# Performance work log

Measured on AMD Instinct MI355X. Metric: run time of the kernel, lower is better.

The kernel has to match this reference:

```python
import jax, jax.numpy as jnp
import numpy as np

N, E, D_IN, H, D_OUT = 50000, 1600000, 256, 128, 64


def setup_inputs() -> dict:
    key = jax.random.key(0)
    ks = jax.random.split(key, 8)
    x = jax.random.normal(ks[0], (N, D_IN), dtype=jnp.float32)
    edge_index = jax.random.randint(ks[1], (2, E), 0, N, dtype=jnp.int64)
    W1 = jax.random.normal(ks[2], (D_IN, H), dtype=jnp.float32) / np.float32(np.sqrt(D_IN))
    b1 = jnp.zeros((H,), jnp.float32)
    W2 = jax.random.normal(ks[3], (H, H), dtype=jnp.float32) / np.float32(np.sqrt(H))
    b2 = jnp.zeros((H,), jnp.float32)
    W3 = jax.random.normal(ks[4], (H, D_OUT), dtype=jnp.float32) / np.float32(np.sqrt(H))
    b3 = jnp.zeros((D_OUT,), jnp.float32)
    return {"x": x, "W1": W1, "b1": b1, "W2": W2, "b2": b2, "W3": W3, "b3": b3,
            "edge_index": edge_index}


def reference(x, W1, b1, W2, b2, W3, b3, edge_index):
    n = x.shape[0]
    # GCN: add self-loops, symmetric normalization D^{-1/2}(A+I)D^{-1/2}
    loop = jnp.arange(n, dtype=edge_index.dtype)
    src = jnp.concatenate([edge_index[0], loop])
    dst = jnp.concatenate([edge_index[1], loop])
    deg = jax.ops.segment_sum(jnp.ones_like(dst, x.dtype), dst, num_segments=n)
    dinv = jnp.where(deg > 0, jax.lax.rsqrt(deg), 0.0).astype(x.dtype)
    norm = dinv[src] * dinv[dst]  # [E+N]

    def gcn_layer(h, W, b):
        h = h @ W                                   # [N, F_out]
        msg = norm[:, None] * h[src]                # gather + scale, [E+N, F_out]
        return jax.ops.segment_sum(msg, dst, num_segments=n) + b

    h = jax.nn.relu(gcn_layer(x, W1, b1))
    h = jax.nn.relu(gcn_layer(h, W2, b2))
    return gcn_layer(h, W3, b3)
```

## Files before the change

### kernel.cpp

```cpp
#include <hip/hip_runtime.h>


constexpr int DIN = 256;
constexpr int HID = 128;
constexpr int DOUT = 64;
constexpr int MAXB = 1024;
constexpr int BSH = 6;
constexpr int EPB = 8192;

typedef unsigned short ushort_t;
typedef unsigned int uint_t;
typedef __attribute__((ext_vector_type(8))) short bf16x8;
typedef __attribute__((ext_vector_type(4))) float f32x4;

__device__ inline ushort_t f2bf(float f) {
  uint_t u = __float_as_uint(f);
  u += 0x7FFF + ((u >> 16) & 1);
  return (ushort_t)(u >> 16);
}
__device__ inline float bf2f(ushort_t b) {
  return __uint_as_float(((uint_t)b) << 16);
}

template <int SH>
__device__ inline uint_t ldrow32(const ushort_t* __restrict__ t, int c, uint_t lb) {
  return *(const uint_t*)((const char*)t + ((((uint_t)c) << SH) | lb));
}
__device__ inline float ldf32(const float* __restrict__ p, int c) {
  return *(const float*)((const char*)p + (((uint_t)c) << 2));
}


__device__ inline void wprep_one(const float* __restrict__ W, ushort_t* __restrict__ Bhi,
                                 ushort_t* __restrict__ Blo, int K, int F, int i) {
  int k = i / F, nn = i % F;
  int t = nn >> 4, s = k >> 5, q = (k >> 3) & 3, j = k & 7;
  int lane = q * 16 + (nn & 15);
  int KS = K >> 5;
  size_t idx = (((size_t)t * KS + s) * 64 + (size_t)lane) * 8 + j;
  float w = W[i];
  ushort_t h = f2bf(w);
  float r = w - bf2f(h);
  Bhi[idx] = h;
  Blo[idx] = f2bf(r);
}


__global__ __launch_bounds__(256) void initprep_kernel(
    int* __restrict__ bucket_total, int iblocks,
    const float* __restrict__ W1, ushort_t* __restrict__ W1hi, ushort_t* __restrict__ W1lo,
    const float* __restrict__ W2, ushort_t* __restrict__ W2hi, ushort_t* __restrict__ W2lo,
    const float* __restrict__ W3, ushort_t* __restrict__ W3hi, ushort_t* __restrict__ W3lo) {
  if ((int)blockIdx.x < iblocks) {
    int i = blockIdx.x * 256 + threadIdx.x;
    if (i < MAXB) bucket_total[i] = 0;
  } else {
    int idx = ((int)blockIdx.x - iblocks) * 256 + threadIdx.x;
    constexpr int S1 = DIN * HID;
    constexpr int S2 = S1 + HID * HID;
    constexpr int S3 = S2 + HID * DOUT;
    if (idx < S1) wprep_one(W1, W1hi, W1lo, DIN, HID, idx);
    else if (idx < S2) wprep_one(W2, W2hi, W2lo, HID, HID, idx - S1);
    else if (idx < S3) wprep_one(W3, W3hi, W3lo, HID, DOUT, idx - S2);
  }
}


__global__ __launch_bounds__(256) void bin_kernel(const int* __restrict__ dst, int e,
    int nbuckets, int* __restrict__ bucket_total, int* __restrict__ block_base) {
  __shared__ int h[MAXB];
  int tid = threadIdx.x;
  for (int i = tid; i < nbuckets; i += 256) h[i] = 0;
  __syncthreads();
  int base = blockIdx.x * EPB;
  int end = min(base + EPB, e);
  for (int i = base + tid; i < end; i += 256) atomicAdd(&h[dst[i] >> BSH], 1);
  __syncthreads();
  for (int i = tid; i < nbuckets; i += 256) {
    int v = h[i];
    if (v) block_base[(size_t)blockIdx.x * nbuckets + i] = atomicAdd(&bucket_total[i], v);
  }
}


__global__ __launch_bounds__(256) void scan_buckets_kernel(const int* __restrict__ total,
    int* __restrict__ base, int nb) {
  __shared__ int sums[256];
  int t = threadIdx.x;
  int a[4];
  int ls = 0;
#pragma unroll
  for (int k = 0; k < 4; ++k) {
    int idx = t * 4 + k;
    a[k] = (idx < nb) ? total[idx] : 0;
    ls += a[k];
  }
  sums[t] = ls;
  __syncthreads();
  for (int off = 1; off < 256; off <<= 1) {
    int u = (t >= off) ? sums[t - off] : 0;
    __syncthreads();
    sums[t] += u;
    __syncthreads();
  }
  int run = sums[t] - ls;
#pragma unroll
  for (int k = 0; k < 4; ++k) {
    int idx = t * 4 + k;
    if (idx < nb) base[idx] = run;
    run += a[k];
  }
  if (t == 255) base[nb] = sums[255];
}


template <int K, int F, bool SCALE>
__device__ inline void gemm_mfma_dev(const float* __restrict__ X,
    const ushort_t* __restrict__ Bhi, const ushort_t* __restrict__ Blo,
    const float* __restrict__ dinv, ushort_t* __restrict__ T, int n, int bid) {
  constexpr int NT = F / 16;
  constexpr int KS = K / 32;
  int wave = threadIdx.x >> 6;
  int lane = threadIdx.x & 63;
  int q = lane >> 4;
  int m = lane & 15;
  int arow = bid * 64 + wave * 16 + m;
  bool valid = arow < n;
  const float* xrow = X + (size_t)arow * K;

  f32x4 acc[NT];
#pragma unroll
  for (int t = 0; t < NT; ++t) acc[t] = (f32x4){0.f, 0.f, 0.f, 0.f};

  for (int s = 0; s < KS; ++s) {
    float av[8];
    if (valid) {
      float4 u0 = *(const float4*)(xrow + s * 32 + q * 8);
      float4 u1 = *(const float4*)(xrow + s * 32 + q * 8 + 4);
      av[0] = u0.x; av[1] = u0.y; av[2] = u0.z; av[3] = u0.w;
      av[4] = u1.x; av[5] = u1.y; av[6] = u1.z; av[7] = u1.w;
    } else {
#pragma unroll
      for (int j = 0; j < 8; ++j) av[j] = 0.f;
    }
    bf16x8 ahi, alo;
#pragma unroll
    for (int j = 0; j < 8; ++j) {
      ushort_t h = f2bf(av[j]);
      ahi[j] = (short)h;
      alo[j] = (short)f2bf(av[j] - bf2f(h));
    }
#pragma unroll
    for (int t = 0; t < NT; ++t) {
      size_t boff = (((size_t)t * KS + s) * 64 + (size_t)lane) * 8;
      bf16x8 bh = *(const bf16x8*)(Bhi + boff);
      bf16x8 bl = *(const bf16x8*)(Blo + boff);
      acc[t] = __builtin_amdgcn_mfma_f32_16x16x32_bf16(ahi, bh, acc[t], 0, 0, 0);
      acc[t] = __builtin_amdgcn_mfma_f32_16x16x32_bf16(alo, bh, acc[t], 0, 0, 0);
      acc[t] = __builtin_amdgcn_mfma_f32_16x16x32_bf16(ahi, bl, acc[t], 0, 0, 0);
    }
  }

  int orow_base = bid * 64 + wave * 16 + q * 4;
#pragma unroll
  for (int r = 0; r < 4; ++r) {
    int orow = orow_base + r;
    if (orow >= n) continue;
    float sc = SCALE ? dinv[orow] : 1.0f;
    ushort_t* trow = T + (size_t)orow * F + m;
#pragma unroll
    for (int t = 0; t < NT; ++t) trow[t * 16] = f2bf(sc * acc[t][r]);
  }
}


__global__ __launch_bounds__(256) void fusedA2_kernel(
    const float* __restrict__ X, const ushort_t* __restrict__ Bhi,
    const ushort_t* __restrict__ Blo, ushort_t* __restrict__ T, int n, int gblocks,
    const int* __restrict__ src, const int* __restrict__ dst,
    const int* __restrict__ bucket_base, const int* __restrict__ block_base,
    uint_t* __restrict__ binned, int e, int nbuckets) {
  if ((int)blockIdx.x < gblocks) {
    gemm_mfma_dev<DIN, HID, false>(X, Bhi, Blo, nullptr, T, n, blockIdx.x);
  } else {
    __shared__ int rkh[MAXB];
    __shared__ int cbase[MAXB];
    int tid = threadIdx.x;
    int blk = (int)blockIdx.x - gblocks;
    for (int i = tid; i < nbuckets; i += 256) {
      rkh[i] = 0;
      cbase[i] = bucket_base[i] + block_base[(size_t)blk * nbuckets + i];
    }
    __syncthreads();
    int base = blk * EPB;
    int end = min(base + EPB, e);
    for (int i = base + tid; i < end; i += 256) {
      int d = dst[i];
      int s = src[i];
      int b = d >> BSH;
      int r = atomicAdd(&rkh[b], 1);
      binned[cbase[b] + r] = ((uint_t)d << 16) | (uint_t)s;
    }
  }
}


__global__ __launch_bounds__(256) void csr_kernel(const uint_t* __restrict__ binned,
    const int* __restrict__ bucket_base, int n, int* __restrict__ row_start,
    int* __restrict__ deg, float* __restrict__ dinv, int* __restrict__ col) {
  __shared__ int cnt[64];
  __shared__ int rk[64];
  __shared__ int rs[64];
  __shared__ int ebs[2];
  int tid = threadIdx.x;
  int b = blockIdx.x;
  int node0 = b << BSH;
  if (tid < 64) { cnt[tid] = 0; rk[tid] = 0; }
  if (tid == 0) { ebs[0] = bucket_base[b]; ebs[1] = bucket_base[b + 1]; }
  __syncthreads();
  int ebase = ebs[0];
  int esz = ebs[1] - ebase;
  for (int i = tid; i < esz; i += 256)
    atomicAdd(&cnt[(int)(binned[ebase + i] >> 16) - node0], 1);
  __syncthreads();
  if (tid < 64) {
    int v = cnt[tid];
    int inc = v;
#pragma unroll
    for (int off = 1; off < 64; off <<= 1) {
      int u = __shfl_up(inc, off, 64);
      if (tid >= off) inc += u;
    }
    rs[tid] = inc - v;
    int node = node0 + tid;
    if (node < n) {
      deg[node] = v + 1;
      dinv[node] = rsqrtf((float)(v + 1));
      row_start[node] = ebase + (inc - v);
    }
  }
  __syncthreads();
  for (int i = tid; i < esz; i += 256) {
    uint_t p = binned[ebase + i];
    int l = (int)(p >> 16) - node0;
    int r = atomicAdd(&rk[l], 1);
    col[ebase + rs[l] + r] = (int)(p & 0xFFFFu);
  }
}


template <int FOUT, bool GD>
__global__ __launch_bounds__(256) void spmm_gemm_kernel(
    const ushort_t* __restrict__ t, const int* __restrict__ row_start,
    const int* __restrict__ deg, const int* __restrict__ col,
    const float* __restrict__ dinv, const float* __restrict__ bias,
    const ushort_t* __restrict__ Bhi, const ushort_t* __restrict__ Blo,
    ushort_t* __restrict__ Tout, int n) {
  constexpr int FIN = 128;
  constexpr int NPB = 8;
  constexpr int LDW = FIN + 4;
  __shared__ float agg[16][LDW];
  int wave = threadIdx.x >> 6;
  int lane = threadIdx.x & 63;
  int tid = threadIdx.x;
  int nb0 = (int)blockIdx.x * NPB;
  uint_t lb = (uint_t)lane << 2;

  {
    float* z = &agg[8][0];
    for (int i = tid; i < 8 * LDW; i += 256) z[i] = 0.f;
  }

  {
    int ln0 = wave * 2;
    int n0 = nb0 + ln0;
    int n1 = n0 + 1;
    bool h0 = n0 < n, h1 = n1 < n;
    int rs0 = h0 ? row_start[n0] : 0, e0 = h0 ? deg[n0] - 1 : 0;
    int rs1 = h1 ? row_start[n1] : 0, e1 = h1 ? deg[n1] - 1 : 0;
    float di0 = h0 ? dinv[n0] : 0.f;
    float di1 = h1 ? dinv[n1] : 0.f;
    float bx = bias[2 * lane], by = bias[2 * lane + 1];
    float ax0 = 0.f, ay0 = 0.f, ax1 = 0.f, ay1 = 0.f;
    if (h0) {
      uint_t s0 = ldrow32<8>(t, n0, lb);
      ax0 = bf2f((ushort_t)(s0 & 0xFFFF)); ay0 = bf2f((ushort_t)(s0 >> 16));
      if constexpr (GD) { ax0 *= di0; ay0 *= di0; }
    }
    if (h1) {
      uint_t s1 = ldrow32<8>(t, n1, lb);
      ax1 = bf2f((ushort_t)(s1 & 0xFFFF)); ay1 = bf2f((ushort_t)(s1 >> 16));
      if constexpr (GD) { ax1 *= di1; ay1 *= di1; }
    }
    int p0 = rs0, q0 = rs0 + e0;
    int p1 = rs1, q1 = rs1 + e1;
    while (p0 + 4 <= q0 && p1 + 4 <= q1) {
      int c[8];
      uint_t v[8];
      float dc[8];
#pragma unroll
      for (int j = 0; j < 4; ++j) { c[j] = col[p0 + j]; c[4 + j] = col[p1 + j]; }
#pragma unroll
      for (int j = 0; j < 8; ++j) {
        v[j] = ldrow32<8>(t, c[j], lb);
        if constexpr (GD) dc[j] = ldf32(dinv, c[j]);
      }
#pragma unroll
      for (int j = 0; j < 4; ++j) {
        if constexpr (GD) {
          ax0 = fmaf(dc[j], bf2f((ushort_t)(v[j] & 0xFFFF)), ax0);
          ay0 = fmaf(dc[j], bf2f((ushort_t)(v[j] >> 16)), ay0);
          ax1 = fmaf(dc[4 + j], bf2f((ushort_t)(v[4 + j] & 0xFFFF)), ax1);
          ay1 = fmaf(dc[4 + j], bf2f((ushort_t)(v[4 + j] >> 16)), ay1);
        } else {
          ax0 += bf2f((ushort_t)(v[j] & 0xFFFF));
          ay0 += bf2f((ushort_t)(v[j] >> 16));
          ax1 += bf2f((ushort_t)(v[4 + j] & 0xFFFF));
          ay1 += bf2f((ushort_t)(v[4 + j] >> 16));
        }
      }
      p0 += 4; p1 += 4;
    }
    for (; p0 + 4 <= q0; p0 += 4) {
      int c[4]; uint_t v[4]; float dc[4];
#pragma unroll
      for (int j = 0; j < 4; ++j) c[j] = col[p0 + j];
#pragma unroll
      for (int j = 0; j < 4; ++j) {
        v[j] = ldrow32<8>(t, c[j], lb);
        if constexpr (GD) dc[j] = ldf32(dinv, c[j]);
      }
#pragma unroll
      for (int j = 0; j < 4; ++j) {
        if constexpr (GD) {
          ax0 = fmaf(dc[j], bf2f((ushort_t)(v[j] & 0xFFFF)), ax0);
          ay0 = fmaf(dc[j], bf2f((ushort_t)(v[j] >> 16)), ay0);
        } else {
          ax0 += bf2f((ushort_t)(v[j] & 0xFFFF)); ay0 += bf2f((ushort_t)(v[j] >> 16));
        }
      }
    }
    for (; p0 < q0; ++p0) {
      int c = col[p0];
      uint_t v = ldrow32<8>(t, c, lb);
      if constexpr (GD) {
        float d = ldf32(dinv, c);
        ax0 = fmaf(d, bf2f((ushort_t)(v & 0xFFFF)), ax0);
        ay0 = fmaf(d, bf2f((ushort_t)(v >> 16)), ay0);
      } else {
        ax0 += bf2f((ushort_t)(v & 0xFFFF)); ay0 += bf2f((ushort_t)(v >> 16));
      }
    }
    for (; p1 + 4 <= q1; p1 += 4) {
      int c[4]; uint_t v[4]; float dc[4];
#pragma unroll
      for (int j = 0; j < 4; ++j) c[j] = col[p1 + j];
#pragma unroll
      for (int j = 0; j < 4; ++j) {
        v[j] = ldrow32<8>(t, c[j], lb);
        if constexpr (GD) dc[j] = ldf32(dinv, c[j]);
      }
#pragma unroll
      for (int j = 0; j < 4; ++j) {
        if constexpr (GD) {
          ax1 = fmaf(dc[j], bf2f((ushort_t)(v[j] & 0xFFFF)), ax1);
          ay1 = fmaf(dc[j], bf2f((ushort_t)(v[j] >> 16)), ay1);
        } else {
          ax1 += bf2f((ushort_t)(v[j] & 0xFFFF)); ay1 += bf2f((ushort_t)(v[j] >> 16));
        }
      }
    }
    for (; p1 < q1; ++p1) {
      int c = col[p1];
      uint_t v = ldrow32<8>(t, c, lb);
      if constexpr (GD) {
        float d = ldf32(dinv, c);
        ax1 = fmaf(d, bf2f((ushort_t)(v & 0xFFFF)), ax1);
        ay1 = fmaf(d, bf2f((ushort_t)(v >> 16)), ay1);
      } else {
        ax1 += bf2f((ushort_t)(v & 0xFFFF)); ay1 += bf2f((ushort_t)(v >> 16));
      }
    }
    float2 o0, o1;
    o0.x = h0 ? fmaxf(fmaf(di0, ax0, bx), 0.f) : 0.f;
    o0.y = h0 ? fmaxf(fmaf(di0, ay0, by), 0.f) : 0.f;
    o1.x = h1 ? fmaxf(fmaf(di1, ax1, bx), 0.f) : 0.f;
    o1.y = h1 ? fmaxf(fmaf(di1, ay1, by), 0.f) : 0.f;
    *(float2*)&agg[ln0][2 * lane] = o0;
    *(float2*)&agg[ln0 + 1][2 * lane] = o1;
  }
  __syncthreads();

  constexpr int NT = FOUT / 16;
  constexpr int KS = FIN / 32;
  constexpr int NTW = NT / 4;
  int q = lane >> 4, m = lane & 15;
  f32x4 acc[NTW];
#pragma unroll
  for (int tt = 0; tt < NTW; ++tt) acc[tt] = (f32x4){0.f, 0.f, 0.f, 0.f};
  const float* arow = &agg[m][0];
#pragma unroll
  for (int s = 0; s < KS; ++s) {
    float4 u0 = *(const float4*)(arow + s * 32 + q * 8);
    float4 u1 = *(const float4*)(arow + s * 32 + q * 8 + 4);
    float av[8];
    av[0] = u0.x; av[1] = u0.y; av[2] = u0.z; av[3] = u0.w;
    av[4] = u1.x; av[5] = u1.y; av[6] = u1.z; av[7] = u1.w;
    bf16x8 ahi, alo;
#pragma unroll
    for (int j = 0; j < 8; ++j) {
      ushort_t h = f2bf(av[j]);
      ahi[j] = (short)h;
      alo[j] = (short)f2bf(av[j] - bf2f(h));
    }
#pragma unroll
    for (int tt = 0; tt < NTW; ++tt) {
      int tg = wave * NTW + tt;
      size_t boff = (((size_t)tg * KS + s) * 64 + (size_t)lane) * 8;
      bf16x8 bh = *(const bf16x8*)(Bhi + boff);
      bf16x8 bl = *(const bf16x8*)(Blo + boff);
      acc[tt] = __builtin_amdgcn_mfma_f32_16x16x32_bf16(ahi, bh, acc[tt], 0, 0, 0);
      acc[tt] = __builtin_amdgcn_mfma_f32_16x16x32_bf16(alo, bh, acc[tt], 0, 0, 0);
      acc[tt] = __builtin_amdgcn_mfma_f32_16x16x32_bf16(ahi, bl, acc[tt], 0, 0, 0);
    }
  }
#pragma unroll
  for (int r = 0; r < 4; ++r) {
    int row = q * 4 + r;
    if (row >= NPB) continue;
    int orow = nb0 + row;
    if (orow >= n) continue;
    float sc = dinv[orow];
    ushort_t* trow = Tout + (size_t)orow * FOUT + m;
#pragma unroll
    for (int tt = 0; tt < NTW; ++tt)
      trow[(wave * NTW + tt) * 16] = f2bf(sc * acc[tt][r]);
  }
}


__global__ __launch_bounds__(256) void spmm64_kernel(const ushort_t* __restrict__ t,
    const int* __restrict__ row_start, const int* __restrict__ deg,
    const int* __restrict__ col, const float* __restrict__ dinv,
    const float* __restrict__ bias, float* __restrict__ out, int n) {
  int gw = (int)((blockIdx.x * 256u + threadIdx.x) >> 6);
  int lane = threadIdx.x & 63;
  int half = lane >> 5;
  int hl = lane & 31;
  int n0 = gw * 2;
  if (n0 >= n) return;
  int node = n0 + half;
  bool valid = node < n;
  int vnode = valid ? node : n0;
  int rs = row_start[vnode];
  int e  = valid ? (deg[vnode] - 1) : 0;
  float di = dinv[vnode];
  uint_t lb = (uint_t)hl << 2;

  uint_t su = ldrow32<7>(t, vnode, lb);
  float ax = bf2f((ushort_t)(su & 0xFFFF));
  float ay = bf2f((ushort_t)(su >> 16));

  int emax = max(e, __shfl_xor(e, 32));
  for (int k = 0; k < emax; k += 4) {
    int c[4];
    uint_t v[4];
#pragma unroll
    for (int j = 0; j < 4; ++j) {
      int on = (k + j) < e;
      c[j] = col[on ? (rs + k + j) : 0];
    }
#pragma unroll
    for (int j = 0; j < 4; ++j) v[j] = ldrow32<7>(t, c[j], lb);
#pragma unroll
    for (int j = 0; j < 4; ++j) {
      if ((k + j) < e) {
        ax += bf2f((ushort_t)(v[j] & 0xFFFF));
        ay += bf2f((ushort_t)(v[j] >> 16));
      }
    }
  }
  if (valid) {
    float bx = bias[2 * hl], by = bias[2 * hl + 1];
    ax = fmaf(di, ax, bx);
    ay = fmaf(di, ay, by);
    float2 o;
    o.x = ax;
    o.y = ay;
    *(float2*)(out + (size_t)node * DOUT + 2 * hl) = o;
  }
}


extern "C" void kernel_launch(void* const* d_in, const int* in_sizes, int n_in,
                              void* d_out, int out_size, void* d_ws, size_t ws_size,
                              hipStream_t stream) {
  const float* x  = (const float*)d_in[0];
  const float* W1 = (const float*)d_in[1];
  const float* b1 = (const float*)d_in[2];
  const float* W2 = (const float*)d_in[3];
  const float* b2 = (const float*)d_in[4];
  const float* W3 = (const float*)d_in[5];
  const float* b3 = (const float*)d_in[6];
  const int* ei   = (const int*)d_in[7];

  int n = in_sizes[0] / DIN;
  int e = in_sizes[7] / 2;
  const int* src = ei;
  const int* dst = ei + e;

  char* ws = (char*)d_ws;
  size_t off = 0;
  auto alloc = [&](size_t bytes) -> void* {
    off = (off + 255) & ~(size_t)255;
    void* p = ws + off;
    off += bytes;
    return p;
  };
  int nbuckets = (n + 63) >> BSH;
  int nbin = (e + EPB - 1) / EPB;

  int*      bucket_total = (int*)alloc((size_t)MAXB * 4);
  int*      bucket_base  = (int*)alloc((size_t)(MAXB + 1) * 4);
  int*      block_base   = (int*)alloc((size_t)nbin * nbuckets * 4);
  uint_t*   binned       = (uint_t*)alloc((size_t)e * 4);
  int*      deg          = (int*)alloc((size_t)n * 4);
  float*    dinv         = (float*)alloc((size_t)n * 4);
  int*      row_start    = (int*)alloc((size_t)n * 4);
  int*      col          = (int*)alloc((size_t)e * 4);
  ushort_t* Ta           = (ushort_t*)alloc((size_t)n * HID * 2);
  ushort_t* Tb           = (ushort_t*)alloc((size_t)n * HID * 2);
  ushort_t* W1hi         = (ushort_t*)alloc((size_t)DIN * HID * 2);
  ushort_t* W1lo         = (ushort_t*)alloc((size_t)DIN * HID * 2);
  ushort_t* W2hi         = (ushort_t*)alloc((size_t)HID * HID * 2);
  ushort_t* W2lo         = (ushort_t*)alloc((size_t)HID * HID * 2);
  ushort_t* W3hi         = (ushort_t*)alloc((size_t)HID * DOUT * 2);
  ushort_t* W3lo         = (ushort_t*)alloc((size_t)HID * DOUT * 2);
  (void)ws_size;

  int gemm_blocks = (n + 63) / 64;
  int sg_blocks = (n + 7) / 8;
  int nwaves = (n + 1) / 2;
  int spmm_blocks = (nwaves + 3) / 4;
  constexpr int WPREP_TOTAL = DIN * HID + HID * HID + HID * DOUT;
  int wblocks = (WPREP_TOTAL + 255) / 256;
  int iblocks = MAXB / 256;

  initprep_kernel<<<iblocks + wblocks, 256, 0, stream>>>(
      bucket_total, iblocks,
      W1, W1hi, W1lo, W2, W2hi, W2lo, W3, W3hi, W3lo);
  bin_kernel<<<nbin, 256, 0, stream>>>(dst, e, nbuckets, bucket_total, block_base);
  scan_buckets_kernel<<<1, 256, 0, stream>>>(bucket_total, bucket_base, nbuckets);
  fusedA2_kernel<<<gemm_blocks + nbin, 256, 0, stream>>>(
      x, W1hi, W1lo, Ta, n, gemm_blocks,
      src, dst, bucket_base, block_base, binned, e, nbuckets);
  csr_kernel<<<nbuckets, 256, 0, stream>>>(binned, bucket_base, n, row_start, deg, dinv, col);

  spmm_gemm_kernel<HID, true><<<sg_blocks, 256, 0, stream>>>(
      Ta, row_start, deg, col, dinv, b1, W2hi, W2lo, Tb, n);
  spmm_gemm_kernel<DOUT, false><<<sg_blocks, 256, 0, stream>>>(
      Tb, row_start, deg, col, dinv, b2, W3hi, W3lo, Ta, n);
  spmm64_kernel<<<spmm_blocks, 256, 0, stream>>>(
      Ta, row_start, deg, col, dinv, b3, (float*)d_out, n);
}
```

Measured before the change: 356.8 us.

## Prescale layer-1 features by dinv in CSR kernel and deepen gather unrolling

The CSR build kernel now also multiplies each row of the first-layer transformed features (bf16) by its node's dinv, writing back in place. This removes the per-edge dinv gather from the first SpMM, so the GD template path goes away. The SpMM loops also gain an 8-wide paired unroll, and the final SpMM drops the lockstep half-wave loop in favour of per-node trip counts with 8 loads in flight. The tradeoff is an extra read/write pass over the layer-1 features and one additional bf16 rounding of the prescaled values.

```diff
diff --git a/kernel.cpp b/kernel.cpp
--- a/kernel.cpp
+++ b/kernel.cpp
@@ -25,9 +25,6 @@
 template <int SH>
 __device__ inline uint_t ldrow32(const ushort_t* __restrict__ t, int c, uint_t lb) {
   return *(const uint_t*)((const char*)t + ((((uint_t)c) << SH) | lb));
-}
-__device__ inline float ldf32(const float* __restrict__ p, int c) {
-  return *(const float*)((const char*)p + (((uint_t)c) << 2));
 }
 
 
@@ -207,10 +204,12 @@
 
 __global__ __launch_bounds__(256) void csr_kernel(const uint_t* __restrict__ binned,
     const int* __restrict__ bucket_base, int n, int* __restrict__ row_start,
-    int* __restrict__ deg, float* __restrict__ dinv, int* __restrict__ col) {
+    int* __restrict__ deg, float* __restrict__ dinv, int* __restrict__ col,
+    ushort_t* __restrict__ Ta) {
   __shared__ int cnt[64];
   __shared__ int rk[64];
   __shared__ int rs[64];
+  __shared__ float sdinv[64];
   __shared__ int ebs[2];
   int tid = threadIdx.x;
   int b = blockIdx.x;
@@ -232,10 +231,12 @@
       if (tid >= off) inc += u;
     }
     rs[tid] = inc - v;
+    float di = rsqrtf((float)(v + 1));
+    sdinv[tid] = di;
     int node = node0 + tid;
     if (node < n) {
       deg[node] = v + 1;
-      dinv[node] = rsqrtf((float)(v + 1));
+      dinv[node] = di;
       row_start[node] = ebase + (inc - v);
     }
   }
@@ -246,10 +247,28 @@
     int r = atomicAdd(&rk[l], 1);
     col[ebase + rs[l] + r] = (int)(p & 0xFFFFu);
   }
-}
-
-
-template <int FOUT, bool GD>
+  int nrows = min(64, n - node0);
+  if (nrows > 0) {
+    uint4* tw = (uint4*)Ta + ((size_t)node0 << 4);
+    int nv4 = nrows << 4;
+    for (int i = tid; i < nv4; i += 256) {
+      float sc = sdinv[i >> 4];
+      uint4 w = tw[i];
+      uint_t ww[4] = {w.x, w.y, w.z, w.w};
+#pragma unroll
+      for (int j = 0; j < 4; ++j) {
+        float lo = sc * bf2f((ushort_t)(ww[j] & 0xFFFF));
+        float hi = sc * bf2f((ushort_t)(ww[j] >> 16));
+        ww[j] = (uint_t)f2bf(lo) | ((uint_t)f2bf(hi) << 16);
+      }
+      w.x = ww[0]; w.y = ww[1]; w.z = ww[2]; w.w = ww[3];
+      tw[i] = w;
+    }
+  }
+}
+
+
+template <int FOUT>
 __global__ __launch_bounds__(256) void spmm_gemm_kernel(
     const ushort_t* __restrict__ t, const int* __restrict__ row_start,
     const int* __restrict__ deg, const int* __restrict__ col,
@@ -285,101 +304,74 @@
     if (h0) {
       uint_t s0 = ldrow32<8>(t, n0, lb);
       ax0 = bf2f((ushort_t)(s0 & 0xFFFF)); ay0 = bf2f((ushort_t)(s0 >> 16));
-      if constexpr (GD) { ax0 *= di0; ay0 *= di0; }
     }
     if (h1) {
       uint_t s1 = ldrow32<8>(t, n1, lb);
       ax1 = bf2f((ushort_t)(s1 & 0xFFFF)); ay1 = bf2f((ushort_t)(s1 >> 16));
-      if constexpr (GD) { ax1 *= di1; ay1 *= di1; }
     }
     int p0 = rs0, q0 = rs0 + e0;
     int p1 = rs1, q1 = rs1 + e1;
+    while (p0 + 8 <= q0 && p1 + 8 <= q1) {
+      int c[16];
+      uint_t v[16];
+#pragma unroll
+      for (int j = 0; j < 8; ++j) { c[j] = col[p0 + j]; c[8 + j] = col[p1 + j]; }
+#pragma unroll
+      for (int j = 0; j < 16; ++j) v[j] = ldrow32<8>(t, c[j], lb);
+#pragma unroll
+      for (int j = 0; j < 8; ++j) {
+        ax0 += bf2f((ushort_t)(v[j] & 0xFFFF));
+        ay0 += bf2f((ushort_t)(v[j] >> 16));
+        ax1 += bf2f((ushort_t)(v[8 + j] & 0xFFFF));
+        ay1 += bf2f((ushort_t)(v[8 + j] >> 16));
+      }
+      p0 += 8; p1 += 8;
+    }
     while (p0 + 4 <= q0 && p1 + 4 <= q1) {
       int c[8];
       uint_t v[8];
-      float dc[8];
 #pragma unroll
       for (int j = 0; j < 4; ++j) { c[j] = col[p0 + j]; c[4 + j] = col[p1 + j]; }
 #pragma unroll
-      for (int j = 0; j < 8; ++j) {
-        v[j] = ldrow32<8>(t, c[j], lb);
-        if constexpr (GD) dc[j] = ldf32(dinv, c[j]);
-      }
+      for (int j = 0; j < 8; ++j) v[j] = ldrow32<8>(t, c[j], lb);
 #pragma unroll
       for (int j = 0; j < 4; ++j) {
-        if constexpr (GD) {
-          ax0 = fmaf(dc[j], bf2f((ushort_t)(v[j] & 0xFFFF)), ax0);
-          ay0 = fmaf(dc[j], bf2f((ushort_t)(v[j] >> 16)), ay0);
-          ax1 = fmaf(dc[4 + j], bf2f((ushort_t)(v[4 + j] & 0xFFFF)), ax1);
-          ay1 = fmaf(dc[4 + j], bf2f((ushort_t)(v[4 + j] >> 16)), ay1);
-        } else {
-          ax0 += bf2f((ushort_t)(v[j] & 0xFFFF));
-          ay0 += bf2f((ushort_t)(v[j] >> 16));
-          ax1 += bf2f((ushort_t)(v[4 + j] & 0xFFFF));
-          ay1 += bf2f((ushort_t)(v[4 + j] >> 16));
-        }
+        ax0 += bf2f((ushort_t)(v[j] & 0xFFFF));
+        ay0 += bf2f((ushort_t)(v[j] >> 16));
+        ax1 += bf2f((ushort_t)(v[4 + j] & 0xFFFF));
+        ay1 += bf2f((ushort_t)(v[4 + j] >> 16));
       }
       p0 += 4; p1 += 4;
     }
     for (; p0 + 4 <= q0; p0 += 4) {
-      int c[4]; uint_t v[4]; float dc[4];
+      int c[4]; uint_t v[4];
 #pragma unroll
       for (int j = 0; j < 4; ++j) c[j] = col[p0 + j];
 #pragma unroll
+      for (int j = 0; j < 4; ++j) v[j] = ldrow32<8>(t, c[j], lb);
+#pragma unroll
       for (int j = 0; j < 4; ++j) {
-        v[j] = ldrow32<8>(t, c[j], lb);
-        if constexpr (GD) dc[j] = ldf32(dinv, c[j]);
+        ax0 += bf2f((ushort_t)(v[j] & 0xFFFF)); ay0 += bf2f((ushort_t)(v[j] >> 16));
       }
+    }
+    for (; p0 < q0; ++p0) {
+      uint_t v = ldrow32<8>(t, col[p0], lb);
+      ax0 += bf2f((ushort_t)(v & 0xFFFF)); ay0 += bf2f((ushort_t)(v >> 16));
+    }
+    for (; p1 + 4 <= q1; p1 += 4) {
+      int c[4]; uint_t v[4];
+#pragma unroll
+      for (int j = 0; j < 4; ++j) c[j] = col[p1 + j];
+#pragma unroll
+      for (int j = 0; j < 4; ++j) v[j] = ldrow32<8>(t, c[j], lb);
 #pragma unroll
       for (int j = 0; j < 4; ++j) {
-        if constexpr (GD) {
-          ax0 = fmaf(dc[j], bf2f((ushort_t)(v[j] & 0xFFFF)), ax0);
-          ay0 = fmaf(dc[j], bf2f((ushort_t)(v[j] >> 16)), ay0);
-        } else {
-          ax0 += bf2f((ushort_t)(v[j] & 0xFFFF)); ay0 += bf2f((ushort_t)(v[j] >> 16));
-        }
+        ax1 += bf2f((ushort_t)(v[j] & 0xFFFF)); ay1 += bf2f((ushort_t)(v[j] >> 16));
       }
     }
-    for (; p0 < q0; ++p0) {
-      int c = col[p0];
-      uint_t v = ldrow32<8>(t, c, lb);
-      if constexpr (GD) {
-        float d = ldf32(dinv, c);
-        ax0 = fmaf(d, bf2f((ushort_t)(v & 0xFFFF)), ax0);
-        ay0 = fmaf(d, bf2f((ushort_t)(v >> 16)), ay0);
-      } else {
-        ax0 += bf2f((ushort_t)(v & 0xFFFF)); ay0 += bf2f((ushort_t)(v >> 16));
-      }
-    }
-    for (; p1 + 4 <= q1; p1 += 4) {
-      int c[4]; uint_t v[4]; float dc[4];
-#pragma unroll
-      for (int j = 0; j < 4; ++j) c[j] = col[p1 + j];
-#pragma unroll
-      for (int j = 0; j < 4; ++j) {
-        v[j] = ldrow32<8>(t, c[j], lb);
-        if constexpr (GD) dc[j] = ldf32(dinv, c[j]);
-      }
-#pragma unroll
-      for (int j = 0; j < 4; ++j) {
-        if constexpr (GD) {
-          ax1 = fmaf(dc[j], bf2f((ushort_t)(v[j] & 0xFFFF)), ax1);
-          ay1 = fmaf(dc[j], bf2f((ushort_t)(v[j] >> 16)), ay1);
-        } else {
-          ax1 += bf2f((ushort_t)(v[j] & 0xFFFF)); ay1 += bf2f((ushort_t)(v[j] >> 16));
-        }
-      }
-    }
     for (; p1 < q1; ++p1) {
-      int c = col[p1];
-      uint_t v = ldrow32<8>(t, c, lb);
-      if constexpr (GD) {
-        float d = ldf32(dinv, c);
-        ax1 = fmaf(d, bf2f((ushort_t)(v & 0xFFFF)), ax1);
-        ay1 = fmaf(d, bf2f((ushort_t)(v >> 16)), ay1);
-      } else {
-        ax1 += bf2f((ushort_t)(v & 0xFFFF)); ay1 += bf2f((ushort_t)(v >> 16));
-      }
+      uint_t v = ldrow32<8>(t, col[p1], lb);
+      ax1 += bf2f((ushort_t)(v & 0xFFFF)); ay1 += bf2f((ushort_t)(v >> 16));
     }
     float2 o0, o1;
     o0.x = h0 ? fmaxf(fmaf(di0, ax0, bx), 0.f) : 0.f;
@@ -461,19 +453,15 @@
   float ax = bf2f((ushort_t)(su & 0xFFFF));
   float ay = bf2f((ushort_t)(su >> 16));
 
-  int emax = max(e, __shfl_xor(e, 32));
-  for (int k = 0; k < emax; k += 4) {
-    int c[4];
-    uint_t v[4];
-#pragma unroll
-    for (int j = 0; j < 4; ++j) {
-      int on = (k + j) < e;
-      c[j] = col[on ? (rs + k + j) : 0];
-    }
-#pragma unroll
-    for (int j = 0; j < 4; ++j) v[j] = ldrow32<7>(t, c[j], lb);
-#pragma unroll
-    for (int j = 0; j < 4; ++j) {
+  for (int k = 0; k < e; k += 8) {
+    int c[8];
+    uint_t v[8];
+#pragma unroll
+    for (int j = 0; j < 8; ++j) c[j] = col[(k + j) < e ? (rs + k + j) : rs];
+#pragma unroll
+    for (int j = 0; j < 8; ++j) v[j] = ldrow32<7>(t, c[j], lb);
+#pragma unroll
+    for (int j = 0; j < 8; ++j) {
       if ((k + j) < e) {
         ax += bf2f((ushort_t)(v[j] & 0xFFFF));
         ay += bf2f((ushort_t)(v[j] >> 16));
@@ -554,11 +542,12 @@
   fusedA2_kernel<<<gemm_blocks + nbin, 256, 0, stream>>>(
       x, W1hi, W1lo, Ta, n, gemm_blocks,
       src, dst, bucket_base, block_base, binned, e, nbuckets);
-  csr_kernel<<<nbuckets, 256, 0, stream>>>(binned, bucket_base, n, row_start, deg, dinv, col);
-
-  spmm_gemm_kernel<HID, true><<<sg_blocks, 256, 0, stream>>>(
+  csr_kernel<<<nbuckets, 256, 0, stream>>>(binned, bucket_base, n, row_start,
+                                           deg, dinv, col, Ta);
+
+  spmm_gemm_kernel<HID><<<sg_blocks, 256, 0, stream>>>(
       Ta, row_start, deg, col, dinv, b1, W2hi, W2lo, Tb, n);
-  spmm_gemm_kernel<DOUT, false><<<sg_blocks, 256, 0, stream>>>(
+  spmm_gemm_kernel<DOUT><<<sg_blocks, 256, 0, stream>>>(
       Tb, row_start, deg, col, dinv, b2, W3hi, W3lo, Ta, n);
   spmm64_kernel<<<spmm_blocks, 256, 0, stream>>>(
       Ta, row_start, deg, col, dinv, b3, (float*)d_out, n);
```

Result: faster. 333.8 us (-6.4%).
